# Kernel tuning notes

Measured on AMD Instinct MI355X. Metric: run time of the kernel, lower is better.

## Reference

```python
import jax, jax.numpy as jnp
import numpy as np
import math

D_MODEL, N_HEADS, D_FF = 512, 8, 2048
B, S = 4, 2048
EPS = 1e-6


def _layernorm(x, alpha, bias):
    # Faithful to the torch module: std is unbiased (ddof=1) and eps is added to std, not var.
    m = jnp.mean(x, axis=-1, keepdims=True)
    s = jnp.std(x, axis=-1, keepdims=True, ddof=1)
    return alpha * (x - m) / (s + EPS) + bias


def setup_inputs() -> dict:
    key = jax.random.key(0)
    ks = jax.random.split(key, 16)
    d, f = D_MODEL, D_FF
    sd = 1.0 / math.sqrt(d)
    sf = 1.0 / math.sqrt(f)
    return {
        "x": jax.random.normal(ks[0], (B, S, d), jnp.float32),
        "wq": jax.random.normal(ks[1], (d, d), jnp.float32) * sd,
        "bq": jnp.zeros((d,), jnp.float32),
        "wk": jax.random.normal(ks[2], (d, d), jnp.float32) * sd,
        "bk": jnp.zeros((d,), jnp.float32),
        "wv": jax.random.normal(ks[3], (d, d), jnp.float32) * sd,
        "bv": jnp.zeros((d,), jnp.float32),
        "wo": jax.random.normal(ks[4], (d, d), jnp.float32) * sd,
        "bo": jnp.zeros((d,), jnp.float32),
        "w1": jax.random.normal(ks[5], (d, f), jnp.float32) * sd,
        "b1": jnp.zeros((f,), jnp.float32),
        "w2": jax.random.normal(ks[6], (f, d), jnp.float32) * sf,
        "b2": jnp.zeros((d,), jnp.float32),
        "ln1_a": jnp.ones((d,), jnp.float32),
        "ln1_b": jnp.zeros((d,), jnp.float32),
        "ln2_a": jnp.ones((d,), jnp.float32),
        "ln2_b": jnp.zeros((d,), jnp.float32),
    }


def reference(x, wq, bq, wk, bk, wv, bv, wo, bo, w1, b1, w2, b2, ln1_a, ln1_b, ln2_a, ln2_b):
    b, s, d = x.shape
    h, dk = N_HEADS, d // N_HEADS
    # QKV projections -> [b, h, s, dk]
    q = (x @ wq + bq).reshape(b, s, h, dk).transpose(0, 2, 1, 3)
    k = (x @ wk + bk).reshape(b, s, h, dk).transpose(0, 2, 1, 3)
    v = (x @ wv + bv).reshape(b, s, h, dk).transpose(0, 2, 1, 3)
    # Manual scaled-dot-product attention (no mask in EncoderBlock path)
    scores = jnp.einsum("bhqd,bhkd->bhqk", q, k) / jnp.sqrt(jnp.float32(dk))
    probs = jax.nn.softmax(scores, axis=-1)
    attn = jnp.einsum("bhqk,bhkd->bhqd", probs, v)
    concat = attn.transpose(0, 2, 1, 3).reshape(b, s, d)
    mha_out = concat @ wo + bo
    # Residual + LayerNorm 1
    y = _layernorm(x + mha_out, ln1_a, ln1_b)
    # FFN + Residual + LayerNorm 2
    ff = jax.nn.relu(y @ w1 + b1) @ w2 + b2
    return _layernorm(y + ff, ln2_a, ln2_b)
```

## Files before the change

### kernel.cpp

```cpp
#include <hip/hip_runtime.h>
#include <hip/hip_bf16.h>


typedef __bf16 bf16;
typedef __bf16 bf16x4 __attribute__((ext_vector_type(4)));
typedef __bf16 bf16x8 __attribute__((ext_vector_type(8)));
typedef float  f32x4  __attribute__((ext_vector_type(4)));

#define NBATCH 4
#define SEQ    2048
#define DMODEL 512
#define NHEADS 8
#define DHEAD  64
#define DFF    2048
#define MTOT   (NBATCH * SEQ)
#define WS_NEED 73416704u
#define QSCALE (0.125f * 1.44269504f)

__device__ __forceinline__ f32x4 mfma16(bf16x8 a, bf16x8 b, f32x4 c) {
    return __builtin_amdgcn_mfma_f32_16x16x32_bf16(a, b, c, 0, 0, 0);
}

__device__ __forceinline__ void lds16(const bf16* g, bf16* l) {
    __builtin_amdgcn_global_load_lds(
        (const __attribute__((address_space(1))) void*)g,
        (__attribute__((address_space(3))) void*)l, 16, 0, 0);
}

__device__ __forceinline__ float scrub(float f) {
    return (fabsf(f) < 1e30f) ? f : 0.f;
}

__global__ void sentinel_kernel(bf16* out) {
    out[threadIdx.x] = (bf16)1000.0f;
}

__global__ __launch_bounds__(256) void prep_kernel(
        const float* x,
        const float* wq, const float* wk, const float* wv, const float* wo,
        const float* w1, const float* w2,
        const float* bq, const float* bk, const float* bv, const float* bo,
        const float* b1, const float* b2,
        const float* l1a, const float* l1b, const float* l2a, const float* l2b,
        bf16* __restrict__ xcv,
        bf16* __restrict__ wT, bf16* __restrict__ w1T, bf16* __restrict__ w2T,
        bf16* __restrict__ prm) {
    __shared__ bf16 tile[32][33];
    int b = blockIdx.x;
    if (b < 4096) {
        int i = (b * 256 + threadIdx.x) * 4;
        float4 f = *(const float4*)(x + i);
        bf16x4 o = {(bf16)scrub(f.x), (bf16)scrub(f.y),
                    (bf16)scrub(f.z), (bf16)scrub(f.w)};
        *(bf16x4*)(xcv + i) = o;
        return;
    }
    if (b < 4106) {
        int pb = b - 4096;
        const float* srcs[10] = {bq, bk, bv, bo, b1, b2, l1a, l1b, l2a, l2b};
        const int len[10] = {512,512,512,512,2048,512,512,512,512,512};
        const int dst[10] = {0,512,1024,1536,2048,4096,4608,5120,5632,6144};
        const float* s = srcs[pb];
        bf16* d = prm + dst[pb];
        for (int i = threadIdx.x; i < len[pb]; i += 256)
            d[i] = (bf16)scrub(s[i]);
        return;
    }
    const float* in; bf16* out; int K, N, bx, by;
    if (b < 5130) {
        int idx = b - 4106, z = idx >> 8, rem = idx & 255;
        const float* srcs[4] = {wq, wk, wv, wo};
        in = srcs[z]; out = wT + (size_t)z * 262144;
        K = 512; N = 512; bx = rem & 15; by = rem >> 4;
    } else if (b < 6154) {
        int idx = b - 5130;
        in = w1; out = w1T; K = 512; N = 2048; bx = idx & 63; by = idx >> 6;
    } else {
        int idx = b - 6154;
        in = w2; out = w2T; K = 2048; N = 512; bx = idx & 15; by = idx >> 4;
    }
    int tx = threadIdx.x & 31, ty = threadIdx.x >> 5;
    int n0 = bx * 32, k0 = by * 32;
#pragma unroll
    for (int i = 0; i < 4; i++) {
        int kl = ty * 4 + i;
        tile[kl][tx] = (bf16)scrub(in[(size_t)(k0 + kl) * N + n0 + tx]);
    }
    __syncthreads();
#pragma unroll
    for (int i = 0; i < 4; i++) {
        int nl = ty * 4 + i;
        out[(size_t)(n0 + nl) * K + k0 + tx] = tile[tx][nl];
    }
}

template <bool RELU>
__global__ __launch_bounds__(256) void gemm_bt(
        const bf16* __restrict__ A, const bf16* __restrict__ BT,
        const bf16* __restrict__ bias, bf16* __restrict__ Cout,
        int M, int N, int K) {
    constexpr int BM = 128, BN = 128;
    __shared__ __align__(16) bf16 As0[BM * 32], As1[BM * 32];
    __shared__ __align__(16) bf16 Bs0[BN * 32], Bs1[BN * 32];

    int tid  = threadIdx.x;
    int wid  = tid >> 6, lane = tid & 63;
    int quad = lane >> 4, l15 = lane & 15;
    int mb = blockIdx.x * BM, nb = blockIdx.y * BN;
    int wm = (wid >> 1) * 64, wn = (wid & 1) * 64;

    f32x4 acc[4][4] = {};

    int c0 = wid * 128 + lane, c1 = c0 + 64;
    int ar0 = c0 >> 2, ac0 = (c0 & 3) * 8;
    int ar1 = c1 >> 2, ac1 = (c1 & 3) * 8;
    int o0 = wid * 1024, o1 = wid * 1024 + 512;

    for (int k0 = 0; k0 < K; k0 += 64) {
        __syncthreads();
        lds16(&A [(size_t)(mb + ar0) * K + k0 + ac0],      &As0[o0]);
        lds16(&A [(size_t)(mb + ar1) * K + k0 + ac1],      &As0[o1]);
        lds16(&A [(size_t)(mb + ar0) * K + k0 + 32 + ac0], &As1[o0]);
        lds16(&A [(size_t)(mb + ar1) * K + k0 + 32 + ac1], &As1[o1]);
        lds16(&BT[(size_t)(nb + ar0) * K + k0 + ac0],      &Bs0[o0]);
        lds16(&BT[(size_t)(nb + ar1) * K + k0 + ac1],      &Bs0[o1]);
        lds16(&BT[(size_t)(nb + ar0) * K + k0 + 32 + ac0], &Bs1[o0]);
        lds16(&BT[(size_t)(nb + ar1) * K + k0 + 32 + ac1], &Bs1[o1]);
        __syncthreads();

        bf16x8 af[4], bfr[4];
#pragma unroll
        for (int i = 0; i < 4; i++)
            af[i] = *(const bf16x8*)&As0[(wm + i * 16 + l15) * 32 + quad * 8];
#pragma unroll
        for (int j = 0; j < 4; j++)
            bfr[j] = *(const bf16x8*)&Bs0[(wn + j * 16 + l15) * 32 + quad * 8];
#pragma unroll
        for (int i = 0; i < 4; i++)
#pragma unroll
            for (int j = 0; j < 4; j++)
                acc[i][j] = mfma16(af[i], bfr[j], acc[i][j]);
#pragma unroll
        for (int i = 0; i < 4; i++)
            af[i] = *(const bf16x8*)&As1[(wm + i * 16 + l15) * 32 + quad * 8];
#pragma unroll
        for (int j = 0; j < 4; j++)
            bfr[j] = *(const bf16x8*)&Bs1[(wn + j * 16 + l15) * 32 + quad * 8];
#pragma unroll
        for (int i = 0; i < 4; i++)
#pragma unroll
            for (int j = 0; j < 4; j++)
                acc[i][j] = mfma16(af[i], bfr[j], acc[i][j]);
    }

#pragma unroll
    for (int j = 0; j < 4; j++) {
        int n = nb + wn + j * 16 + l15;
        float bv = (float)bias[n];
#pragma unroll
        for (int i = 0; i < 4; i++) {
            int mBase = mb + wm + i * 16 + quad * 4;
#pragma unroll
            for (int r = 0; r < 4; r++) {
                float v = acc[i][j][r] + bv;
                if (RELU) v = v > 0.f ? v : 0.f;
                Cout[(size_t)(mBase + r) * N + n] = (bf16)v;
            }
        }
    }
}

template <bool RELU>
__global__ __launch_bounds__(256) void gemm_bt64(
        const bf16* __restrict__ A, const bf16* __restrict__ BT,
        const bf16* __restrict__ bias, bf16* __restrict__ Cout,
        int M, int N, int K) {
    constexpr int BM = 64, BN = 128;
    __shared__ __align__(16) bf16 As0[BM * 32], As1[BM * 32];
    __shared__ __align__(16) bf16 Bs0[BN * 32], Bs1[BN * 32];

    int tid  = threadIdx.x;
    int wid  = tid >> 6, lane = tid & 63;
    int quad = lane >> 4, l15 = lane & 15;
    int mb = blockIdx.x * BM, nb = blockIdx.y * BN;
    int wm = (wid >> 1) * 32, wn = (wid & 1) * 64;

    f32x4 acc[2][4] = {};

    int cA = wid * 64 + lane;
    int arA = cA >> 2, acA = (cA & 3) * 8;
    int cB0 = wid * 128 + lane, cB1 = cB0 + 64;
    int br0 = cB0 >> 2, bc0 = (cB0 & 3) * 8;
    int br1 = cB1 >> 2, bc1 = (cB1 & 3) * 8;

    for (int k0 = 0; k0 < K; k0 += 64) {
        __syncthreads();
        lds16(&A [(size_t)(mb + arA) * K + k0 + acA],      &As0[wid * 512]);
        lds16(&A [(size_t)(mb + arA) * K + k0 + 32 + acA], &As1[wid * 512]);
        lds16(&BT[(size_t)(nb + br0) * K + k0 + bc0],      &Bs0[wid * 1024]);
        lds16(&BT[(size_t)(nb + br1) * K + k0 + bc1],      &Bs0[wid * 1024 + 512]);
        lds16(&BT[(size_t)(nb + br0) * K + k0 + 32 + bc0], &Bs1[wid * 1024]);
        lds16(&BT[(size_t)(nb + br1) * K + k0 + 32 + bc1], &Bs1[wid * 1024 + 512]);
        __syncthreads();

        bf16x8 a0[2], a1[2], b0[4], b1[4];
#pragma unroll
        for (int i = 0; i < 2; i++) {
            a0[i] = *(const bf16x8*)&As0[(wm + i * 16 + l15) * 32 + quad * 8];
            a1[i] = *(const bf16x8*)&As1[(wm + i * 16 + l15) * 32 + quad * 8];
        }
#pragma unroll
        for (int j = 0; j < 4; j++) {
            b0[j] = *(const bf16x8*)&Bs0[(wn + j * 16 + l15) * 32 + quad * 8];
            b1[j] = *(const bf16x8*)&Bs1[(wn + j * 16 + l15) * 32 + quad * 8];
        }
#pragma unroll
        for (int i = 0; i < 2; i++)
#pragma unroll
            for (int j = 0; j < 4; j++)
                acc[i][j] = mfma16(a1[i], b1[j], mfma16(a0[i], b0[j], acc[i][j]));
    }

#pragma unroll
    for (int j = 0; j < 4; j++) {
        int n = nb + wn + j * 16 + l15;
        float bv = (float)bias[n];
#pragma unroll
        for (int i = 0; i < 2; i++) {
            int mBase = mb + wm + i * 16 + quad * 4;
#pragma unroll
            for (int r = 0; r < 4; r++) {
                float v = acc[i][j][r] + bv;
                if (RELU) v = v > 0.f ? v : 0.f;
                Cout[(size_t)(mBase + r) * N + n] = (bf16)v;
            }
        }
    }
}

__global__ __launch_bounds__(256) void gemm_qkv(
        const bf16* __restrict__ A, const bf16* __restrict__ BT,
        const bf16* __restrict__ bias,
        bf16* __restrict__ Cq, bf16* __restrict__ Ck, bf16* __restrict__ Cv,
        int M, int N, int K) {
    constexpr int BM = 128, BN = 128;
    __shared__ __align__(16) bf16 As0[BM * 32], As1[BM * 32];
    __shared__ __align__(16) bf16 Bs0[BN * 32], Bs1[BN * 32];
    __shared__ __align__(16) bf16 Ts[128 * 136];

    int tid  = threadIdx.x;
    int wid  = tid >> 6, lane = tid & 63;
    int quad = lane >> 4, l15 = lane & 15;
    int mb = blockIdx.x * BM, nb = blockIdx.y * BN;
    int wm = (wid >> 1) * 64, wn = (wid & 1) * 64;

    f32x4 acc[4][4] = {};

    int c0 = wid * 128 + lane, c1 = c0 + 64;
    int ar0 = c0 >> 2, ac0 = (c0 & 3) * 8;
    int ar1 = c1 >> 2, ac1 = (c1 & 3) * 8;
    int o0 = wid * 1024, o1 = wid * 1024 + 512;

    for (int k0 = 0; k0 < K; k0 += 64) {
        __syncthreads();
        lds16(&A [(size_t)(mb + ar0) * K + k0 + ac0],      &As0[o0]);
        lds16(&A [(size_t)(mb + ar1) * K + k0 + ac1],      &As0[o1]);
        lds16(&A [(size_t)(mb + ar0) * K + k0 + 32 + ac0], &As1[o0]);
        lds16(&A [(size_t)(mb + ar1) * K + k0 + 32 + ac1], &As1[o1]);
        lds16(&BT[(size_t)(nb + ar0) * K + k0 + ac0],      &Bs0[o0]);
        lds16(&BT[(size_t)(nb + ar1) * K + k0 + ac1],      &Bs0[o1]);
        lds16(&BT[(size_t)(nb + ar0) * K + k0 + 32 + ac0], &Bs1[o0]);
        lds16(&BT[(size_t)(nb + ar1) * K + k0 + 32 + ac1], &Bs1[o1]);
        __syncthreads();

        bf16x8 af[4], bfr[4];
#pragma unroll
        for (int i = 0; i < 4; i++)
            af[i] = *(const bf16x8*)&As0[(wm + i * 16 + l15) * 32 + quad * 8];
#pragma unroll
        for (int j = 0; j < 4; j++)
            bfr[j] = *(const bf16x8*)&Bs0[(wn + j * 16 + l15) * 32 + quad * 8];
#pragma unroll
        for (int i = 0; i < 4; i++)
#pragma unroll
            for (int j = 0; j < 4; j++)
                acc[i][j] = mfma16(af[i], bfr[j], acc[i][j]);
#pragma unroll
        for (int i = 0; i < 4; i++)
            af[i] = *(const bf16x8*)&As1[(wm + i * 16 + l15) * 32 + quad * 8];
#pragma unroll
        for (int j = 0; j < 4; j++)
            bfr[j] = *(const bf16x8*)&Bs1[(wn + j * 16 + l15) * 32 + quad * 8];
#pragma unroll
        for (int i = 0; i < 4; i++)
#pragma unroll
            for (int j = 0; j < 4; j++)
                acc[i][j] = mfma16(af[i], bfr[j], acc[i][j]);
    }

    int reg = nb >> 9;
    if (reg < 2) {
        bf16* C = reg ? Ck : Cq;
        float scl = reg ? 1.0f : QSCALE;
#pragma unroll
        for (int j = 0; j < 4; j++) {
            int n = nb + wn + j * 16 + l15;
            float bv = (float)bias[n];
            int nn = n & 511;
            int h = nn >> 6, dk = nn & 63;
#pragma unroll
            for (int i = 0; i < 4; i++) {
                int mBase = mb + wm + i * 16 + quad * 4;
#pragma unroll
                for (int r = 0; r < 4; r++) {
                    float v = (acc[i][j][r] + bv) * scl;
                    int m = mBase + r;
                    int b = m >> 11, s = m & (SEQ - 1);
                    C[((size_t)(b * NHEADS + h) * SEQ + s) * DHEAD + dk] = (bf16)v;
                }
            }
        }
    } else {
#pragma unroll
        for (int j = 0; j < 4; j++) {
            int nl = wn + j * 16 + l15;
            float bv = (float)bias[nb + nl];
#pragma unroll
            for (int i = 0; i < 4; i++) {
                int ml = wm + i * 16 + quad * 4;
                bf16x4 pk;
#pragma unroll
                for (int r = 0; r < 4; r++) pk[r] = (bf16)(acc[i][j][r] + bv);
                *(bf16x4*)&Ts[nl * 136 + ml] = pk;
            }
        }
        __syncthreads();
        int nl = tid >> 1, half = tid & 1;
        int nn = (nb + nl) & 511;
        int h = nn >> 6, dk = nn & 63;
        int bb = mb >> 11, s0 = mb & (SEQ - 1);
        bf16* dst = &Cv[((size_t)(bb * NHEADS + h) * DHEAD + dk) * SEQ + s0 + half * 64];
        const bf16* srcl = &Ts[nl * 136 + half * 64];
#pragma unroll
        for (int v = 0; v < 8; v++)
            *(uint4*)(dst + v * 8) = *(const uint4*)(srcl + v * 8);
    }
}

__global__ __launch_bounds__(256) void attn_kernel(
        const bf16* __restrict__ Q, const bf16* __restrict__ K,
        const bf16* __restrict__ VT, bf16* __restrict__ Out) {
    __shared__ __align__(16) bf16 Pb[4][16 * 72];
    int tid  = threadIdx.x;
    int wid  = tid >> 6, lane = tid & 63;
    int quad = lane >> 4, l15 = lane & 15;
    int bh = blockIdx.y;
    int qb = blockIdx.x * 128 + wid * 32;

    const bf16* Qh = Q  + (size_t)bh * SEQ * DHEAD;
    const bf16* Kh = K  + (size_t)bh * SEQ * DHEAD;
    const bf16* Vh = VT + (size_t)bh * DHEAD * SEQ;

    bf16x8 bQ0[2], bQ1[2];
#pragma unroll
    for (int c = 0; c < 2; c++) {
        const bf16* qp = &Qh[(qb + c * 16 + l15) * DHEAD + quad * 8];
        bQ0[c] = *(const bf16x8*)qp;
        bQ1[c] = *(const bf16x8*)(qp + 32);
    }

    float lrow[2] = {0.f, 0.f};
    f32x4 Oacc[2][4] = {};

    const bf16* kp0 = &Kh[(size_t)(0 * 16 + l15) * DHEAD + quad * 8];
    const bf16* kp1 = &Kh[(size_t)(1 * 16 + l15) * DHEAD + quad * 8];
    const bf16* kp2 = &Kh[(size_t)(2 * 16 + l15) * DHEAD + quad * 8];
    const bf16* kp3 = &Kh[(size_t)(3 * 16 + l15) * DHEAD + quad * 8];
    const bf16* vp0 = &Vh[(size_t)(0 * 16 + l15) * SEQ + quad * 8];
    const bf16* vp1 = &Vh[(size_t)(1 * 16 + l15) * SEQ + quad * 8];
    const bf16* vp2 = &Vh[(size_t)(2 * 16 + l15) * SEQ + quad * 8];
    const bf16* vp3 = &Vh[(size_t)(3 * 16 + l15) * SEQ + quad * 8];

    for (int it = 0; it < SEQ / 64; it++) {
        bf16x8 aK0[4], aK1[4], bV0[4], bV1[4];
        aK0[0] = *(const bf16x8*)kp0;  aK1[0] = *(const bf16x8*)(kp0 + 32);
        aK0[1] = *(const bf16x8*)kp1;  aK1[1] = *(const bf16x8*)(kp1 + 32);
        aK0[2] = *(const bf16x8*)kp2;  aK1[2] = *(const bf16x8*)(kp2 + 32);
        aK0[3] = *(const bf16x8*)kp3;  aK1[3] = *(const bf16x8*)(kp3 + 32);
        bV0[0] = *(const bf16x8*)vp0;  bV1[0] = *(const bf16x8*)(vp0 + 32);
        bV0[1] = *(const bf16x8*)vp1;  bV1[1] = *(const bf16x8*)(vp1 + 32);
        bV0[2] = *(const bf16x8*)vp2;  bV1[2] = *(const bf16x8*)(vp2 + 32);
        bV0[3] = *(const bf16x8*)vp3;  bV1[3] = *(const bf16x8*)(vp3 + 32);
        kp0 += 64 * DHEAD; kp1 += 64 * DHEAD; kp2 += 64 * DHEAD; kp3 += 64 * DHEAD;
        vp0 += 64;         vp1 += 64;         vp2 += 64;         vp3 += 64;

#pragma unroll
        for (int c = 0; c < 2; c++) {
            f32x4 st[4];
#pragma unroll
            for (int t = 0; t < 4; t++) {
                f32x4 zv = {0.f, 0.f, 0.f, 0.f};
                st[t] = mfma16(aK1[t], bQ1[c], mfma16(aK0[t], bQ0[c], zv));
            }
            bf16* myP = Pb[wid];
#pragma unroll
            for (int t = 0; t < 4; t++) {
                bf16x4 pk;
                float ps = 0.f;
#pragma unroll
                for (int r = 0; r < 4; r++) {
                    float p = __builtin_amdgcn_exp2f(fminf(st[t][r], 60.f));
                    ps += p;
                    pk[r] = (bf16)p;
                }
                lrow[c] += ps;
                *(bf16x4*)&myP[l15 * 72 + t * 16 + quad * 4] = pk;
            }
            bf16x8 aP0 = *(const bf16x8*)&myP[l15 * 72 + quad * 8];
            bf16x8 aP1 = *(const bf16x8*)&myP[l15 * 72 + 32 + quad * 8];
#pragma unroll
            for (int nt = 0; nt < 4; nt++)
                Oacc[c][nt] = mfma16(aP1, bV1[nt],
                                     mfma16(aP0, bV0[nt], Oacc[c][nt]));
        }
    }

    int b = bh >> 3, hd = bh & 7;
#pragma unroll
    for (int c = 0; c < 2; c++) {
        float l = lrow[c];
        l += __shfl_xor(l, 16);
        l += __shfl_xor(l, 32);
        float linv[4];
#pragma unroll
        for (int r = 0; r < 4; r++)
            linv[r] = 1.f / __shfl(l, quad * 4 + r);
#pragma unroll
        for (int nt = 0; nt < 4; nt++)
#pragma unroll
            for (int r = 0; r < 4; r++) {
                int s = qb + c * 16 + quad * 4 + r;
                Out[((size_t)(b * SEQ + s)) * DMODEL + hd * 64 + nt * 16 + l15]
                    = (bf16)(Oacc[c][nt][r] * linv[r]);
            }
    }
}

__global__ __launch_bounds__(256) void ln_kernel(
        const bf16* __restrict__ X, const bf16* __restrict__ T,
        const bf16* __restrict__ Al, const bf16* __restrict__ Bl,
        void* __restrict__ Out, int final_out) {
    int wid = threadIdx.x >> 6, lane = threadIdx.x & 63;
    int row = blockIdx.x * 4 + wid;
    const bf16* xr = X + (size_t)row * DMODEL;
    const bf16* tr = T + (size_t)row * DMODEL;
    bf16x8 xv = *(const bf16x8*)&xr[lane * 8];
    bf16x8 tv = *(const bf16x8*)&tr[lane * 8];
    float v[8];
#pragma unroll
    for (int i = 0; i < 8; i++) v[i] = (float)xv[i] + (float)tv[i];
    float sum = 0.f, sq = 0.f;
#pragma unroll
    for (int i = 0; i < 8; i++) { sum += v[i]; sq += v[i] * v[i]; }
#pragma unroll
    for (int m = 1; m < 64; m <<= 1) {
        sum += __shfl_xor(sum, m);
        sq  += __shfl_xor(sq,  m);
    }
    float mean = sum * (1.f / DMODEL);
    float var  = (sq - DMODEL * mean * mean) * (1.f / (DMODEL - 1));
    var = var > 0.f ? var : 0.f;
    float inv = 1.f / (sqrtf(var) + 1e-6f);
#pragma unroll
    for (int i = 0; i < 8; i++) {
        int c = lane * 8 + i;
        float yv = (float)Al[c] * (v[i] - mean) * inv + (float)Bl[c];
        yv = fminf(fmaxf(yv, -1e4f), 1e4f);
        size_t idx = (size_t)row * DMODEL + c;
        if (final_out) ((float*)Out)[idx] = yv;
        else           ((bf16*)Out)[idx]  = (bf16)yv;
    }
}

extern "C" void kernel_launch(void* const* d_in, const int* in_sizes, int n_in,
                              void* d_out, int out_size, void* d_ws, size_t ws_size,
                              hipStream_t stream) {
    if (ws_size < WS_NEED) {
        sentinel_kernel<<<1, 64, 0, stream>>>((bf16*)d_out);
        return;
    }

    const float* x  = (const float*)d_in[0];
    const float* wq = (const float*)d_in[1],  *bq = (const float*)d_in[2];
    const float* wk = (const float*)d_in[3],  *bk = (const float*)d_in[4];
    const float* wv = (const float*)d_in[5],  *bv = (const float*)d_in[6];
    const float* wo = (const float*)d_in[7],  *bo = (const float*)d_in[8];
    const float* w1 = (const float*)d_in[9],  *b1 = (const float*)d_in[10];
    const float* w2 = (const float*)d_in[11], *b2 = (const float*)d_in[12];
    const float* ln1a = (const float*)d_in[13], *ln1b = (const float*)d_in[14];
    const float* ln2a = (const float*)d_in[15], *ln2b = (const float*)d_in[16];

    char* ws = (char*)d_ws;
    bf16* wT   = (bf16*)(ws + 0);
    bf16* woT  = (bf16*)(ws + 1572864);
    bf16* w1T  = (bf16*)(ws + 2097152);
    bf16* w2T  = (bf16*)(ws + 4194304);
    bf16* xcv  = (bf16*)(ws + 6291456);
    bf16* prm  = (bf16*)(ws + 14680064);
    bf16* regA = (bf16*)(ws + 14696448);
    bf16* regB = (bf16*)(ws + 23085056);
    bf16* regC = (bf16*)(ws + 31473664);
    bf16* ff1  = (bf16*)(ws + 39862272);
    bf16* aout = (bf16*)d_out;

    bf16 *pbq = prm, *pbo = prm + 1536;
    bf16 *pb1 = prm + 2048, *pb2 = prm + 4096;
    bf16 *pl1a = prm + 4608, *pl1b = prm + 5120;
    bf16 *pl2a = prm + 5632, *pl2b = prm + 6144;

    prep_kernel<<<7178, 256, 0, stream>>>(x, wq, wk, wv, wo, w1, w2,
                                          bq, bk, bv, bo, b1, b2,
                                          ln1a, ln1b, ln2a, ln2b,
                                          xcv, wT, w1T, w2T, prm);

    gemm_qkv<<<dim3(64, 12), 256, 0, stream>>>(xcv, wT, pbq,
                                               regA, regB, regC,
                                               MTOT, 3 * DMODEL, DMODEL);

    attn_kernel<<<dim3(SEQ / 128, NBATCH * NHEADS), 256, 0, stream>>>(
        regA, regB, regC, aout);

    gemm_bt64<false><<<dim3(128, 4), 256, 0, stream>>>(aout, woT, pbo, regA,
                                                       MTOT, DMODEL, DMODEL);

    ln_kernel<<<MTOT / 4, 256, 0, stream>>>(xcv, regA, pl1a, pl1b, regB, 0);

    gemm_bt<true ><<<dim3(64, 16), 256, 0, stream>>>(regB, w1T, pb1, ff1,
                                                     MTOT, DFF, DMODEL);
    gemm_bt64<false><<<dim3(128, 4), 256, 0, stream>>>(ff1, w2T, pb2, regA,
                                                       MTOT, DMODEL, DFF);

    ln_kernel<<<MTOT / 4, 256, 0, stream>>>(regB, regA, pl2a, pl2b, d_out, 1);
}
```

Baseline: 344.8 us.

## Double-buffer K/V register loads, compute row sums via MFMA, swizzle block order

Result: no change. 348.5 us (+1.1%).

```diff
diff --git a/kernel.cpp b/kernel.cpp
--- a/kernel.cpp
+++ b/kernel.cpp
@@ -354,8 +354,11 @@
     int tid  = threadIdx.x;
     int wid  = tid >> 6, lane = tid & 63;
     int quad = lane >> 4, l15 = lane & 15;
-    int bh = blockIdx.y;
-    int qb = blockIdx.x * 128 + wid * 32;
+
+    int lin = blockIdx.y * 16 + blockIdx.x;
+    lin = (lin & 7) * 64 + (lin >> 3);
+    int bh = lin >> 4;
+    int qb = (lin & 15) * 128 + wid * 32;
 
     const bf16* Qh = Q  + (size_t)bh * SEQ * DHEAD;
     const bf16* Kh = K  + (size_t)bh * SEQ * DHEAD;
@@ -369,72 +372,80 @@
         bQ1[c] = *(const bf16x8*)(qp + 32);
     }
 
-    float lrow[2] = {0.f, 0.f};
+    bf16x8 vONE;
+#pragma unroll
+    for (int i = 0; i < 8; i++) vONE[i] = (bf16)1.0f;
+
+    f32x4 lacc[2] = {};
     f32x4 Oacc[2][4] = {};
 
-    const bf16* kp0 = &Kh[(size_t)(0 * 16 + l15) * DHEAD + quad * 8];
-    const bf16* kp1 = &Kh[(size_t)(1 * 16 + l15) * DHEAD + quad * 8];
-    const bf16* kp2 = &Kh[(size_t)(2 * 16 + l15) * DHEAD + quad * 8];
-    const bf16* kp3 = &Kh[(size_t)(3 * 16 + l15) * DHEAD + quad * 8];
-    const bf16* vp0 = &Vh[(size_t)(0 * 16 + l15) * SEQ + quad * 8];
-    const bf16* vp1 = &Vh[(size_t)(1 * 16 + l15) * SEQ + quad * 8];
-    const bf16* vp2 = &Vh[(size_t)(2 * 16 + l15) * SEQ + quad * 8];
-    const bf16* vp3 = &Vh[(size_t)(3 * 16 + l15) * SEQ + quad * 8];
-
-    for (int it = 0; it < SEQ / 64; it++) {
-        bf16x8 aK0[4], aK1[4], bV0[4], bV1[4];
-        aK0[0] = *(const bf16x8*)kp0;  aK1[0] = *(const bf16x8*)(kp0 + 32);
-        aK0[1] = *(const bf16x8*)kp1;  aK1[1] = *(const bf16x8*)(kp1 + 32);
-        aK0[2] = *(const bf16x8*)kp2;  aK1[2] = *(const bf16x8*)(kp2 + 32);
-        aK0[3] = *(const bf16x8*)kp3;  aK1[3] = *(const bf16x8*)(kp3 + 32);
-        bV0[0] = *(const bf16x8*)vp0;  bV1[0] = *(const bf16x8*)(vp0 + 32);
-        bV0[1] = *(const bf16x8*)vp1;  bV1[1] = *(const bf16x8*)(vp1 + 32);
-        bV0[2] = *(const bf16x8*)vp2;  bV1[2] = *(const bf16x8*)(vp2 + 32);
-        bV0[3] = *(const bf16x8*)vp3;  bV1[3] = *(const bf16x8*)(vp3 + 32);
-        kp0 += 64 * DHEAD; kp1 += 64 * DHEAD; kp2 += 64 * DHEAD; kp3 += 64 * DHEAD;
-        vp0 += 64;         vp1 += 64;         vp2 += 64;         vp3 += 64;
-
-#pragma unroll
-        for (int c = 0; c < 2; c++) {
-            f32x4 st[4];
-#pragma unroll
-            for (int t = 0; t < 4; t++) {
-                f32x4 zv = {0.f, 0.f, 0.f, 0.f};
-                st[t] = mfma16(aK1[t], bQ1[c], mfma16(aK0[t], bQ0[c], zv));
-            }
-            bf16* myP = Pb[wid];
-#pragma unroll
-            for (int t = 0; t < 4; t++) {
-                bf16x4 pk;
-                float ps = 0.f;
-#pragma unroll
-                for (int r = 0; r < 4; r++) {
-                    float p = __builtin_amdgcn_exp2f(fminf(st[t][r], 60.f));
-                    ps += p;
-                    pk[r] = (bf16)p;
-                }
-                lrow[c] += ps;
-                *(bf16x4*)&myP[l15 * 72 + t * 16 + quad * 4] = pk;
-            }
-            bf16x8 aP0 = *(const bf16x8*)&myP[l15 * 72 + quad * 8];
-            bf16x8 aP1 = *(const bf16x8*)&myP[l15 * 72 + 32 + quad * 8];
-#pragma unroll
-            for (int nt = 0; nt < 4; nt++)
-                Oacc[c][nt] = mfma16(aP1, bV1[nt],
-                                     mfma16(aP0, bV0[nt], Oacc[c][nt]));
-        }
-    }
+    int kOff = l15 * DHEAD + quad * 8;
+    int vOff = l15 * SEQ   + quad * 8;
+
+    bf16x8 AK0[4], AK1[4], AV0[4], AV1[4];
+    bf16x8 BK0[4], BK1[4], BV0[4], BV1[4];
+
+    const bf16* kb = Kh;
+    const bf16* vb = Vh;
+
+#define LOADF(P, KB, VB)                                                   \
+    _Pragma("unroll")                                                      \
+    for (int t = 0; t < 4; t++) {                                          \
+        const bf16* kp_ = (KB) + t * 16 * DHEAD + kOff;                    \
+        P##K0[t] = *(const bf16x8*)kp_;                                    \
+        P##K1[t] = *(const bf16x8*)(kp_ + 32);                             \
+        const bf16* vp_ = (VB) + t * 16 * SEQ + vOff;                      \
+        P##V0[t] = *(const bf16x8*)vp_;                                    \
+        P##V1[t] = *(const bf16x8*)(vp_ + 32);                             \
+    }
+
+#define COMPUTE(P)                                                         \
+    _Pragma("unroll")                                                      \
+    for (int c = 0; c < 2; c++) {                                          \
+        f32x4 st[4];                                                       \
+        _Pragma("unroll")                                                  \
+        for (int t = 0; t < 4; t++) {                                      \
+            f32x4 zv = {0.f, 0.f, 0.f, 0.f};                               \
+            st[t] = mfma16(P##K1[t], bQ1[c],                               \
+                           mfma16(P##K0[t], bQ0[c], zv));                  \
+        }                                                                  \
+        bf16* myP = Pb[wid];                                               \
+        _Pragma("unroll")                                                  \
+        for (int t = 0; t < 4; t++) {                                      \
+            bf16x4 pk;                                                     \
+            _Pragma("unroll")                                              \
+            for (int r = 0; r < 4; r++)                                    \
+                pk[r] = (bf16)__builtin_amdgcn_exp2f(fminf(st[t][r], 60.f));\
+            *(bf16x4*)&myP[l15 * 72 + t * 16 + quad * 4] = pk;             \
+        }                                                                  \
+         \
+        bf16x8 aP0 = *(const bf16x8*)&myP[l15 * 72 + quad * 8];            \
+        bf16x8 aP1 = *(const bf16x8*)&myP[l15 * 72 + 32 + quad * 8];       \
+        _Pragma("unroll")                                                  \
+        for (int nt = 0; nt < 4; nt++)                                     \
+            Oacc[c][nt] = mfma16(aP1, P##V1[nt],                           \
+                                 mfma16(aP0, P##V0[nt], Oacc[c][nt]));     \
+        lacc[c] = mfma16(aP1, vONE, mfma16(aP0, vONE, lacc[c]));           \
+    }
+
+    LOADF(A, kb, vb);
+    for (int it = 0; it < SEQ / 64; it += 2) {
+        LOADF(B, kb + 64 * DHEAD, vb + 64);
+        COMPUTE(A);
+        kb += 128 * DHEAD; vb += 128;
+        if (it + 2 < SEQ / 64) LOADF(A, kb, vb);
+        COMPUTE(B);
+    }
+#undef LOADF
+#undef COMPUTE
 
     int b = bh >> 3, hd = bh & 7;
 #pragma unroll
     for (int c = 0; c < 2; c++) {
-        float l = lrow[c];
-        l += __shfl_xor(l, 16);
-        l += __shfl_xor(l, 32);
         float linv[4];
 #pragma unroll
         for (int r = 0; r < 4; r++)
-            linv[r] = 1.f / __shfl(l, quad * 4 + r);
+            linv[r] = 1.f / lacc[c][r];
 #pragma unroll
         for (int nt = 0; nt < 4; nt++)
 #pragma unroll
```
